# Performance work log

Hardware: AMD Instinct MI355X
Metric: run time of the kernel (lower is better)

Reference implementation:

```python
import math
import jax, jax.numpy as jnp
import numpy as np

E = 24  # num experts


def layer_norm(x, w, b, eps=1e-6):
    m = x.mean(-1, keepdims=True)
    v = x.var(-1, keepdims=True)
    return (x - m) / jnp.sqrt(v + eps) * w + b


def top2_dispatch(x, Wg, C):
    # x: [S, d] -> combine/dispatch: [S, E, C] (GShard/DeepSpeed top-2 gating)
    logits = x @ Wg                                   # [S, E]
    gates = jax.nn.softmax(logits, axis=-1)
    idx1 = jnp.argmax(gates, axis=-1)
    m1 = jax.nn.one_hot(idx1, E, dtype=x.dtype)       # [S, E]
    masked = jnp.where(m1 > 0, -jnp.inf, logits)
    idx2 = jnp.argmax(masked, axis=-1)
    m2 = jax.nn.one_hot(idx2, E, dtype=x.dtype)
    # position of each token within its expert's capacity buffer
    loc1 = jnp.cumsum(m1, axis=0) - m1
    loc2 = jnp.cumsum(m2, axis=0) - m2 + jnp.sum(m1, axis=0, keepdims=True)
    m1 = m1 * (loc1 < C)                              # drop overflow tokens
    m2 = m2 * (loc2 < C)
    g1 = jnp.sum(gates * m1, axis=-1)
    g2 = jnp.sum(gates * m2, axis=-1)
    denom = jnp.maximum(g1 + g2, 1e-9)
    g1, g2 = g1 / denom, g2 / denom
    p1 = jnp.sum(loc1 * m1, axis=-1).astype(jnp.int32)
    p2 = jnp.sum(loc2 * m2, axis=-1).astype(jnp.int32)
    c1 = g1[:, None, None] * m1[:, :, None] * jax.nn.one_hot(p1, C, dtype=x.dtype)[:, None, :]
    c2 = g2[:, None, None] * m2[:, :, None] * jax.nn.one_hot(p2, C, dtype=x.dtype)[:, None, :]
    combine = c1 + c2                                  # [S, E, C]
    dispatch = (combine > 0).astype(x.dtype)
    return combine, dispatch


def moe_apply(x, combine, dispatch, W, b):
    # dispatch tokens to expert buffers, per-expert GEMM, combine back
    disp = jnp.einsum('sec,sd->ecd', dispatch, x)      # [E, C, d]
    h = jnp.einsum('ecd,edf->ecf', disp, W) + b[:, None, :]
    return jnp.einsum('sec,ecf->sf', combine, h)       # [S, f]


def setup_inputs() -> dict:
    b, seq, d_in, d_hid = 4, 2048, 1024, 4096
    ks = jax.random.split(jax.random.key(0), 6)
    s = 0.02
    return {
        'x': jax.random.normal(ks[0], (b, seq, d_in), dtype=jnp.float32),
        'Wg': jax.random.normal(ks[1], (d_in, E), dtype=jnp.float32) * s,
        'W1': jax.random.normal(ks[2], (E, d_in, d_hid), dtype=jnp.float32) * s,
        'b1': jnp.zeros((E, d_hid), dtype=jnp.float32),
        'W2': jax.random.normal(ks[3], (E, d_hid, d_in), dtype=jnp.float32) * s,
        'b2': jnp.zeros((E, d_in), dtype=jnp.float32),
        'ln_hid_w': jnp.ones((4, d_hid), dtype=jnp.float32),
        'ln_hid_b': jnp.zeros((4, d_hid), dtype=jnp.float32),
        'ln_out_w': jnp.ones((d_in,), dtype=jnp.float32),
        'ln_out_b': jnp.zeros((d_in,), dtype=jnp.float32),
    }


def reference(x, Wg, W1, b1, W2, b2, ln_hid_w, ln_hid_b, ln_out_w, ln_out_b):
    bsz, seq, d = x.shape
    H = 4
    n = seq // H
    S = bsz * n  # tokens per sub-sequence MoE call
    C = math.ceil(2 * S / E)  # top-2 capacity, capacity_factor=1.0
    # b (h n) c -> h (b n) c
    xg = x.reshape(bsz, H, n, d).transpose(1, 0, 2, 3).reshape(H, S, d)

    def per_group(xf, lw, lb):
        combine, dispatch = top2_dispatch(xf, Wg, C)
        h = moe_apply(xf, combine, dispatch, W1, b1)       # [S, d_hid]
        h = layer_norm(h, lw, lb)
        h = jax.nn.relu(h)                                  # dropout = identity (eval)
        return moe_apply(h, combine, dispatch, W2, b2)      # reuse gate_decision

    out = jax.vmap(per_group)(xg, ln_hid_w, ln_hid_b)       # [H, S, d]
    out = out.reshape(H, bsz, n, d).transpose(1, 0, 2, 3).reshape(bsz, seq, d)
    return layer_norm(out + x, ln_out_w, ln_out_b)
```

## Files before the change

### kernel.cpp

```cpp
#include <hip/hip_runtime.h>
#include <cstdint>
#include <cstddef>

#define E_      24
#define D_IN    1024
#define D_HID   4096
#define HGRP    4
#define BSZ     4
#define SEQ     2048
#define NSUB    512
#define S_      2048
#define NTOKG   8192
#define CAP     171
#define MR      768
#define MTILE   3

typedef __attribute__((ext_vector_type(4))) float          f32x4;
typedef __attribute__((ext_vector_type(2))) float          f32x2;
typedef __attribute__((ext_vector_type(4))) unsigned short u16x4;
typedef __attribute__((ext_vector_type(8))) unsigned short u16x8;
typedef __attribute__((ext_vector_type(4))) unsigned int   u32x4;
typedef __attribute__((ext_vector_type(8))) short          s16x8;

__device__ __forceinline__ unsigned short f2bf(float f) {
  unsigned int u = __float_as_uint(f);
  u += 0x7fffu + ((u >> 16) & 1u);
  return (unsigned short)(u >> 16);
}
__device__ __forceinline__ float bf2f(unsigned short v) {
  return __uint_as_float(((unsigned int)v) << 16);
}

__global__ __launch_bounds__(64)
void k_gating(const float* __restrict__ x, const float* __restrict__ Wg,
              int* __restrict__ tokE1, int* __restrict__ tokE2,
              float* __restrict__ tokG1, float* __restrict__ tokG2) {
  int tg = blockIdx.x;
  int h = tg >> 11, s = tg & 2047;
  int bi = s >> 9, ni = s & 511;
  const float* xr = x + ((size_t)bi*SEQ + (size_t)h*NSUB + ni) * D_IN;
  int lane = threadIdx.x;
  float acc[E_];
  #pragma unroll
  for (int e = 0; e < E_; ++e) acc[e] = 0.f;
  #pragma unroll
  for (int it = 0; it < D_IN/256; ++it) {
    f32x4 xv = *(const f32x4*)(xr + it*256 + lane*4);
    #pragma unroll
    for (int j = 0; j < 4; ++j) {
      float xs = xv[j];
      const float* wrow = Wg + (size_t)(it*256 + lane*4 + j) * E_;
      #pragma unroll
      for (int e = 0; e < E_; ++e) acc[e] += xs * wrow[e];
    }
  }
  #pragma unroll
  for (int e = 0; e < E_; ++e) {
    float v = acc[e];
    v += __shfl_xor(v, 32); v += __shfl_xor(v, 16); v += __shfl_xor(v, 8);
    v += __shfl_xor(v, 4);  v += __shfl_xor(v, 2);  v += __shfl_xor(v, 1);
    acc[e] = v;
  }
  if (lane == 0) {
    float mx = acc[0];
    #pragma unroll
    for (int e = 1; e < E_; ++e) mx = fmaxf(mx, acc[e]);
    float den = 0.f;
    #pragma unroll
    for (int e = 0; e < E_; ++e) den += expf(acc[e] - mx);
    int i1 = 0; float v1 = acc[0];
    #pragma unroll
    for (int e = 1; e < E_; ++e) if (acc[e] > v1) { v1 = acc[e]; i1 = e; }
    int i2 = -1; float v2 = -3.4e38f;
    #pragma unroll
    for (int e = 0; e < E_; ++e) if (e != i1 && acc[e] > v2) { v2 = acc[e]; i2 = e; }
    tokE1[tg] = i1; tokE2[tg] = i2;
    tokG1[tg] = expf(v1 - mx) / den;
    tokG2[tg] = expf(v2 - mx) / den;
  }
}

__global__ void k_init_slots(int* __restrict__ slotTok) {
  slotTok[blockIdx.x*256 + threadIdx.x] = -1;
}

__global__ __launch_bounds__(64)
void k_scan(const int* __restrict__ tokE1, const int* __restrict__ tokE2,
            float* __restrict__ tokG1, float* __restrict__ tokG2,
            int* __restrict__ tokP1, int* __restrict__ tokP2,
            int* __restrict__ slotTok) {
  int h = blockIdx.x;
  int lane = threadIdx.x;
  __shared__ int cnt[64][E_];
  __shared__ int tot1[E_];
  const int CH = S_/64;
  const int* e1 = tokE1 + h*S_;
  const int* e2 = tokE2 + h*S_;
  #pragma unroll
  for (int e = 0; e < E_; ++e) cnt[lane][e] = 0;
  __syncthreads();
  for (int k = 0; k < CH; ++k) cnt[lane][e1[lane*CH + k]]++;
  __syncthreads();
  if (lane < E_) {
    int run = 0;
    for (int j = 0; j < 64; ++j) { int t = cnt[j][lane]; cnt[j][lane] = run; run += t; }
    tot1[lane] = run;
  }
  __syncthreads();
  for (int k = 0; k < CH; ++k) {
    int s = lane*CH + k;
    int e = e1[s];
    int p = cnt[lane][e]++;
    int tg = h*S_ + s;
    if (p < CAP) { tokP1[tg] = p; slotTok[e*MR + h*CAP + p] = tg; }
    else         { tokP1[tg] = -1; }
  }
  __syncthreads();
  #pragma unroll
  for (int e = 0; e < E_; ++e) cnt[lane][e] = 0;
  __syncthreads();
  for (int k = 0; k < CH; ++k) cnt[lane][e2[lane*CH + k]]++;
  __syncthreads();
  if (lane < E_) {
    int run = tot1[lane];
    for (int j = 0; j < 64; ++j) { int t = cnt[j][lane]; cnt[j][lane] = run; run += t; }
  }
  __syncthreads();
  for (int k = 0; k < CH; ++k) {
    int s = lane*CH + k;
    int e = e2[s];
    int p = cnt[lane][e]++;
    int tg = h*S_ + s;
    if (p < CAP) { tokP2[tg] = p; slotTok[e*MR + h*CAP + p] = tg; }
    else         { tokP2[tg] = -1; }
  }
  __syncthreads();
  for (int k = 0; k < CH; ++k) {
    int tg = h*S_ + k*64 + lane;
    float g1 = (tokP1[tg] >= 0) ? tokG1[tg] : 0.f;
    float g2 = (tokP2[tg] >= 0) ? tokG2[tg] : 0.f;
    float den = fmaxf(g1 + g2, 1e-9f);
    tokG1[tg] = g1 / den;
    tokG2[tg] = g2 / den;
  }
}

__global__ __launch_bounds__(256)
void k_gather1(const float* __restrict__ x, const int* __restrict__ slotTok,
               unsigned short* __restrict__ A1) {
  int row = blockIdx.x;
  int tok = slotTok[row];
  int t = threadIdx.x;
  int k = t*4;
  int ba = ((k & 63)*2) ^ ((row & 7) << 4);
  char* dst = (char*)A1 + (size_t)row*(D_IN*2) + (size_t)(k >> 6)*128 + ba;
  u16x4 pk;
  if (tok >= 0) {
    int h = tok >> 11, s = tok & 2047;
    int bi = s >> 9, ni = s & 511;
    const float* xr = x + ((size_t)bi*SEQ + (size_t)h*NSUB + ni) * D_IN;
    f32x4 v = *(const f32x4*)(xr + k);
    pk.x = f2bf(v.x); pk.y = f2bf(v.y); pk.z = f2bf(v.z); pk.w = f2bf(v.w);
  } else {
    pk.x = 0; pk.y = 0; pk.z = 0; pk.w = 0;
  }
  *(u16x4*)dst = pk;
}

template<int K, int N>
__global__ __launch_bounds__(512, 4)
void k_gemm(const unsigned short* __restrict__ A, const float* __restrict__ W,
            const float* __restrict__ bias, unsigned short* __restrict__ Out) {
  const int NT = N / 128;
  int cpx = gridDim.x >> 3;
  int lb = blockIdx.x;
  int bid = (lb & 7) * cpx + (lb >> 3);
  int mt  = bid % MTILE;
  int rem = bid / MTILE;
  int nt  = rem % NT;
  int e   = rem / NT;

  const char*  Ab = (const char*)A + ((size_t)e*MR + (size_t)mt*256) * (K*2);
  const float* We = W + (size_t)e*K*N + (size_t)nt*128;

  __shared__ unsigned short As[256*64];
  __shared__ unsigned short Bs[128*64];
  int tid  = threadIdx.x;
  int lane = tid & 63;
  int wid  = tid >> 6;
  int wr = wid >> 1, wc = wid & 1;

  f32x4 acc[4][4];
  #pragma unroll
  for (int i = 0; i < 4; ++i)
    #pragma unroll
    for (int j = 0; j < 4; ++j) acc[i][j] = (f32x4)0.f;

  int bn0 = (tid & 63) * 2;
  int bkh = (tid >> 6) * 8;
  f32x2 bPre[8];

  auto loadB = [&](int kt) {
    const float* p = We + (size_t)(kt*64 + bkh)*N + bn0;
    #pragma unroll
    for (int q = 0; q < 8; ++q) bPre[q] = *(const f32x2*)(p + (size_t)q*N);
  };
  auto storeB = [&]() {
    u16x8 c0, c1;
    #pragma unroll
    for (int q = 0; q < 8; ++q) { c0[q] = f2bf(bPre[q].x); c1[q] = f2bf(bPre[q].y); }
    int r0 = bn0, r1 = bn0 + 1;
    *(u16x8*)((char*)Bs + r0*128 + ((bkh*2) ^ ((r0 & 7) << 4))) = c0;
    *(u16x8*)((char*)Bs + r1*128 + ((bkh*2) ^ ((r1 & 7) << 4))) = c1;
  };
  auto stageA = [&](int kt) {
    #pragma unroll
    for (int i = 0; i < 4; ++i) {
      int L = i*8192 + tid*16;
      const char* src = Ab + (size_t)(L >> 7)*(K*2) + (size_t)kt*128 + (L & 127);
      __builtin_amdgcn_global_load_lds(
          (const __attribute__((address_space(1))) void*)src,
          (__attribute__((address_space(3))) void*)((char*)As + L),
          16, 0, 0);
    }
  };

  const int NKT = K / 64;
  loadB(0);
  for (int kt = 0; kt < NKT; ++kt) {
    __syncthreads();
    stageA(kt);
    storeB();
    __syncthreads();
    if (kt + 1 < NKT) loadB(kt + 1);
    #pragma unroll
    for (int kk = 0; kk < 2; ++kk) {
      s16x8 afr[4], bfr[4];
      int kx2 = (kk*32 + (lane >> 4)*8) * 2;
      #pragma unroll
      for (int i = 0; i < 4; ++i) {
        int row = wr*64 + i*16 + (lane & 15);
        afr[i] = *(const s16x8*)((const char*)As + row*128 + (kx2 ^ ((row & 7) << 4)));
        int col = wc*64 + i*16 + (lane & 15);
        bfr[i] = *(const s16x8*)((const char*)Bs + col*128 + (kx2 ^ ((col & 7) << 4)));
      }
      #pragma unroll
      for (int i = 0; i < 4; ++i)
        #pragma unroll
        for (int j = 0; j < 4; ++j)
          acc[i][j] = __builtin_amdgcn_mfma_f32_16x16x32_bf16(afr[i], bfr[j], acc[i][j], 0, 0, 0);
    }
  }
  #pragma unroll
  for (int j = 0; j < 4; ++j) {
    int col = nt*128 + wc*64 + j*16 + (lane & 15);
    float bv = bias[(size_t)e*N + col];
    #pragma unroll
    for (int i = 0; i < 4; ++i) {
      int rowb = mt*256 + wr*64 + i*16 + (lane >> 4)*4;
      #pragma unroll
      for (int r = 0; r < 4; ++r) {
        float v = acc[i][j][r] + bv;
        Out[(size_t)e*MR*N + (size_t)(rowb + r)*N + col] = f2bf(v);
      }
    }
  }
}

__global__ __launch_bounds__(256)
void k_zero_empty(const int* __restrict__ slotTok, unsigned short* __restrict__ A2) {
  int row = blockIdx.x;
  if (slotTok[row] >= 0) return;
  u32x4 z = (u32x4)0u;
  char* base = (char*)A2 + (size_t)row*(D_HID*2) + threadIdx.x*32;
  *(u32x4*)base = z;
  *(u32x4*)(base + 16) = z;
}

__global__ __launch_bounds__(256)
void k_combine_ln(const unsigned short* __restrict__ H1,
                  const int* __restrict__ tokE1, const int* __restrict__ tokE2,
                  const int* __restrict__ tokP1, const int* __restrict__ tokP2,
                  const float* __restrict__ tokG1, const float* __restrict__ tokG2,
                  const float* __restrict__ lnw, const float* __restrict__ lnb,
                  unsigned short* __restrict__ A2) {
  int tg = blockIdx.x;
  int h = tg >> 11;
  int p1 = tokP1[tg], p2 = tokP2[tg];
  if (p1 < 0 && p2 < 0) return;
  float g1 = tokG1[tg], g2 = tokG2[tg];
  long r1 = (p1 >= 0) ? ((long)tokE1[tg]*MR + h*CAP + p1) : -1;
  long r2 = (p2 >= 0) ? ((long)tokE2[tg]*MR + h*CAP + p2) : -1;
  int t = threadIdx.x;
  float v[16];
  float sum = 0.f, sq = 0.f;
  #pragma unroll
  for (int u = 0; u < 4; ++u) {
    int f = u*1024 + t*4;
    float a0 = 0.f, a1 = 0.f, a2 = 0.f, a3 = 0.f;
    if (r1 >= 0) {
      u16x4 q = *(const u16x4*)(H1 + (size_t)r1*D_HID + f);
      a0 += g1*bf2f(q.x); a1 += g1*bf2f(q.y); a2 += g1*bf2f(q.z); a3 += g1*bf2f(q.w);
    }
    if (r2 >= 0) {
      u16x4 q = *(const u16x4*)(H1 + (size_t)r2*D_HID + f);
      a0 += g2*bf2f(q.x); a1 += g2*bf2f(q.y); a2 += g2*bf2f(q.z); a3 += g2*bf2f(q.w);
    }
    v[u*4+0] = a0; v[u*4+1] = a1; v[u*4+2] = a2; v[u*4+3] = a3;
    sum += a0 + a1 + a2 + a3;
    sq  += a0*a0 + a1*a1 + a2*a2 + a3*a3;
  }
  #pragma unroll
  for (int o = 32; o; o >>= 1) { sum += __shfl_xor(sum, o); sq += __shfl_xor(sq, o); }
  __shared__ float redA[4], redB[4];
  int wid = t >> 6;
  if ((t & 63) == 0) { redA[wid] = sum; redB[wid] = sq; }
  __syncthreads();
  float S = redA[0] + redA[1] + redA[2] + redA[3];
  float Q = redB[0] + redB[1] + redB[2] + redB[3];
  float m = S * (1.f / D_HID);
  float var = Q * (1.f / D_HID) - m*m;
  float rs = rsqrtf(var + 1e-6f);
  #pragma unroll
  for (int u = 0; u < 4; ++u) {
    int f = u*1024 + t*4;
    u16x4 pk;
    float y0 = fmaxf((v[u*4+0]-m)*rs*lnw[h*D_HID+f+0] + lnb[h*D_HID+f+0], 0.f);
    float y1 = fmaxf((v[u*4+1]-m)*rs*lnw[h*D_HID+f+1] + lnb[h*D_HID+f+1], 0.f);
    float y2 = fmaxf((v[u*4+2]-m)*rs*lnw[h*D_HID+f+2] + lnb[h*D_HID+f+2], 0.f);
    float y3 = fmaxf((v[u*4+3]-m)*rs*lnw[h*D_HID+f+3] + lnb[h*D_HID+f+3], 0.f);
    pk.x = f2bf(y0); pk.y = f2bf(y1); pk.z = f2bf(y2); pk.w = f2bf(y3);
    int chunk = f >> 6;
    int ob = (f & 63)*2;
    if (r1 >= 0)
      *(u16x4*)((char*)A2 + (size_t)r1*(D_HID*2) + (size_t)chunk*128 + (ob ^ (((int)r1 & 7) << 4))) = pk;
    if (r2 >= 0)
      *(u16x4*)((char*)A2 + (size_t)r2*(D_HID*2) + (size_t)chunk*128 + (ob ^ (((int)r2 & 7) << 4))) = pk;
  }
}

__global__ __launch_bounds__(256)
void k_final(const unsigned short* __restrict__ H2, const float* __restrict__ x,
             const int* __restrict__ tokE1, const int* __restrict__ tokE2,
             const int* __restrict__ tokP1, const int* __restrict__ tokP2,
             const float* __restrict__ tokG1, const float* __restrict__ tokG2,
             const float* __restrict__ lnw, const float* __restrict__ lnb,
             float* __restrict__ out) {
  int tg = blockIdx.x;
  int h = tg >> 11, s = tg & 2047;
  int bi = s >> 9, ni = s & 511;
  size_t xoff = ((size_t)bi*SEQ + (size_t)h*NSUB + ni) * D_IN;
  int p1 = tokP1[tg], p2 = tokP2[tg];
  float g1 = tokG1[tg], g2 = tokG2[tg];
  int t = threadIdx.x;
  int f = t*4;
  f32x4 xv = *(const f32x4*)(x + xoff + f);
  float v0 = xv.x, v1 = xv.y, v2 = xv.z, v3 = xv.w;
  if (p1 >= 0) {
    size_t r1 = (size_t)tokE1[tg]*MR + h*CAP + p1;
    u16x4 q = *(const u16x4*)(H2 + r1*D_IN + f);
    v0 += g1*bf2f(q.x); v1 += g1*bf2f(q.y); v2 += g1*bf2f(q.z); v3 += g1*bf2f(q.w);
  }
  if (p2 >= 0) {
    size_t r2 = (size_t)tokE2[tg]*MR + h*CAP + p2;
    u16x4 q = *(const u16x4*)(H2 + r2*D_IN + f);
    v0 += g2*bf2f(q.x); v1 += g2*bf2f(q.y); v2 += g2*bf2f(q.z); v3 += g2*bf2f(q.w);
  }
  float sum = v0+v1+v2+v3, sq = v0*v0+v1*v1+v2*v2+v3*v3;
  #pragma unroll
  for (int o = 32; o; o >>= 1) { sum += __shfl_xor(sum, o); sq += __shfl_xor(sq, o); }
  __shared__ float redA[4], redB[4];
  int wid = t >> 6;
  if ((t & 63) == 0) { redA[wid] = sum; redB[wid] = sq; }
  __syncthreads();
  float S = redA[0] + redA[1] + redA[2] + redA[3];
  float Q = redB[0] + redB[1] + redB[2] + redB[3];
  float m = S * (1.f / D_IN);
  float var = Q * (1.f / D_IN) - m*m;
  float rs = rsqrtf(var + 1e-6f);
  f32x4 res;
  res.x = (v0 - m)*rs*lnw[f+0] + lnb[f+0];
  res.y = (v1 - m)*rs*lnw[f+1] + lnb[f+1];
  res.z = (v2 - m)*rs*lnw[f+2] + lnb[f+2];
  res.w = (v3 - m)*rs*lnw[f+3] + lnb[f+3];
  *(f32x4*)(out + xoff + f) = res;
}

extern "C" void kernel_launch(void* const* d_in, const int* in_sizes, int n_in,
                              void* d_out, int out_size, void* d_ws, size_t ws_size,
                              hipStream_t stream) {
  const float* x    = (const float*)d_in[0];
  const float* Wg   = (const float*)d_in[1];
  const float* W1   = (const float*)d_in[2];
  const float* b1   = (const float*)d_in[3];
  const float* W2   = (const float*)d_in[4];
  const float* b2   = (const float*)d_in[5];
  const float* lnhw = (const float*)d_in[6];
  const float* lnhb = (const float*)d_in[7];
  const float* lnow = (const float*)d_in[8];
  const float* lnob = (const float*)d_in[9];
  float* out = (float*)d_out;
  (void)in_sizes; (void)n_in; (void)out_size; (void)ws_size;

  char* ws = (char*)d_ws;
  size_t off = 0;
  auto take = [&](size_t bytes) -> char* {
    char* p = ws + off;
    off += (bytes + 255) & ~(size_t)255;
    return p;
  };
  int*   tokE1 = (int*)take(NTOKG*sizeof(int));
  int*   tokE2 = (int*)take(NTOKG*sizeof(int));
  int*   tokP1 = (int*)take(NTOKG*sizeof(int));
  int*   tokP2 = (int*)take(NTOKG*sizeof(int));
  float* tokG1 = (float*)take(NTOKG*sizeof(float));
  float* tokG2 = (float*)take(NTOKG*sizeof(float));
  int*   slotTok = (int*)take((size_t)E_*MR*sizeof(int));
  unsigned short* A1 = (unsigned short*)take((size_t)E_*MR*D_IN*2);
  unsigned short* H1 = (unsigned short*)take((size_t)E_*MR*D_HID*2);
  unsigned short* A2 = (unsigned short*)take((size_t)E_*MR*D_HID*2);
  unsigned short* H2 = (unsigned short*)take((size_t)E_*MR*D_IN*2);

  k_init_slots<<<dim3(E_*MR/256), dim3(256), 0, stream>>>(slotTok);
  k_gating<<<dim3(NTOKG), dim3(64), 0, stream>>>(x, Wg, tokE1, tokE2, tokG1, tokG2);
  k_scan<<<dim3(HGRP), dim3(64), 0, stream>>>(tokE1, tokE2, tokG1, tokG2, tokP1, tokP2, slotTok);
  k_gather1<<<dim3(E_*MR), dim3(256), 0, stream>>>(x, slotTok, A1);
  k_gemm<D_IN, D_HID><<<dim3(E_*(D_HID/128)*MTILE), dim3(512), 0, stream>>>(A1, W1, b1, H1);
  k_zero_empty<<<dim3(E_*MR), dim3(256), 0, stream>>>(slotTok, A2);
  k_combine_ln<<<dim3(NTOKG), dim3(256), 0, stream>>>(H1, tokE1, tokE2, tokP1, tokP2,
                                                      tokG1, tokG2, lnhw, lnhb, A2);
  k_gemm<D_HID, D_IN><<<dim3(E_*(D_IN/128)*MTILE), dim3(512), 0, stream>>>(A2, W2, b2, H2);
  k_final<<<dim3(NTOKG), dim3(256), 0, stream>>>(H2, x, tokE1, tokE2, tokP1, tokP2,
                                                 tokG1, tokG2, lnow, lnob, out);
}
```

Measured before the change: 812.4 us.

## Double-buffer LDS tiles in expert GEMM with manual waitcnt ping-pong

```diff
diff --git a/kernel.cpp b/kernel.cpp
--- a/kernel.cpp
+++ b/kernel.cpp
@@ -168,7 +168,7 @@
 }
 
 template<int K, int N>
-__global__ __launch_bounds__(512, 4)
+__global__ __launch_bounds__(512)
 void k_gemm(const unsigned short* __restrict__ A, const float* __restrict__ W,
             const float* __restrict__ bias, unsigned short* __restrict__ Out) {
   const int NT = N / 128;
@@ -183,8 +183,10 @@
   const char*  Ab = (const char*)A + ((size_t)e*MR + (size_t)mt*256) * (K*2);
   const float* We = W + (size_t)e*K*N + (size_t)nt*128;
 
-  __shared__ unsigned short As[256*64];
-  __shared__ unsigned short Bs[128*64];
+  __shared__ unsigned short As0[256*64];
+  __shared__ unsigned short As1[256*64];
+  __shared__ unsigned short Bs0[128*64];
+  __shared__ unsigned short Bs1[128*64];
   int tid  = threadIdx.x;
   int lane = tid & 63;
   int wid  = tid >> 6;
@@ -198,22 +200,22 @@
 
   int bn0 = (tid & 63) * 2;
   int bkh = (tid >> 6) * 8;
-  f32x2 bPre[8];
-
-  auto loadB = [&](int kt) {
+  f32x2 bPreA[8], bPreB[8];
+
+  auto loadB = [&](int kt, f32x2* bp) {
     const float* p = We + (size_t)(kt*64 + bkh)*N + bn0;
     #pragma unroll
-    for (int q = 0; q < 8; ++q) bPre[q] = *(const f32x2*)(p + (size_t)q*N);
+    for (int q = 0; q < 8; ++q) bp[q] = *(const f32x2*)(p + (size_t)q*N);
   };
-  auto storeB = [&]() {
+  auto storeB = [&](const f32x2* bp, unsigned short* Bs) {
     u16x8 c0, c1;
     #pragma unroll
-    for (int q = 0; q < 8; ++q) { c0[q] = f2bf(bPre[q].x); c1[q] = f2bf(bPre[q].y); }
+    for (int q = 0; q < 8; ++q) { c0[q] = f2bf(bp[q].x); c1[q] = f2bf(bp[q].y); }
     int r0 = bn0, r1 = bn0 + 1;
     *(u16x8*)((char*)Bs + r0*128 + ((bkh*2) ^ ((r0 & 7) << 4))) = c0;
     *(u16x8*)((char*)Bs + r1*128 + ((bkh*2) ^ ((r1 & 7) << 4))) = c1;
   };
-  auto stageA = [&](int kt) {
+  auto stageA = [&](int kt, unsigned short* As) {
     #pragma unroll
     for (int i = 0; i < 4; ++i) {
       int L = i*8192 + tid*16;
@@ -224,15 +226,7 @@
           16, 0, 0);
     }
   };
-
-  const int NKT = K / 64;
-  loadB(0);
-  for (int kt = 0; kt < NKT; ++kt) {
-    __syncthreads();
-    stageA(kt);
-    storeB();
-    __syncthreads();
-    if (kt + 1 < NKT) loadB(kt + 1);
+  auto compute = [&](const unsigned short* As, const unsigned short* Bs) {
     #pragma unroll
     for (int kk = 0; kk < 2; ++kk) {
       s16x8 afr[4], bfr[4];
@@ -250,6 +244,28 @@
         for (int j = 0; j < 4; ++j)
           acc[i][j] = __builtin_amdgcn_mfma_f32_16x16x32_bf16(afr[i], bfr[j], acc[i][j], 0, 0, 0);
     }
+  };
+
+  const int NKT = K / 64;
+  stageA(0, As0); loadB(0, bPreA);
+  for (int kt = 0; kt < NKT; kt += 2) {
+    stageA(kt + 1, As1);
+    loadB(kt + 1, bPreB);
+    storeB(bPreA, Bs0);
+    asm volatile("s_waitcnt vmcnt(12) lgkmcnt(0)" ::: "memory");
+    __builtin_amdgcn_sched_barrier(0);
+    __builtin_amdgcn_s_barrier();
+    compute(As0, Bs0);
+    __builtin_amdgcn_sched_barrier(0);
+    __builtin_amdgcn_s_barrier();
+    if (kt + 2 < NKT) { stageA(kt + 2, As0); loadB(kt + 2, bPreA); }
+    storeB(bPreB, Bs1);
+    asm volatile("s_waitcnt vmcnt(12) lgkmcnt(0)" ::: "memory");
+    __builtin_amdgcn_sched_barrier(0);
+    __builtin_amdgcn_s_barrier();
+    compute(As1, Bs1);
+    __builtin_amdgcn_sched_barrier(0);
+    __builtin_amdgcn_s_barrier();
   }
   #pragma unroll
   for (int j = 0; j < 4; ++j) {
```

New measurement: 944.8 us. +16.3%, slower.

## Widen expert GEMM tile to 256x256 with double-buffered LDS pipeline

Applied to the files above, without the earlier changes.

```diff
diff --git a/kernel.cpp b/kernel.cpp
--- a/kernel.cpp
+++ b/kernel.cpp
@@ -168,10 +168,10 @@
 }
 
 template<int K, int N>
-__global__ __launch_bounds__(512, 4)
+__global__ __launch_bounds__(512, 2)
 void k_gemm(const unsigned short* __restrict__ A, const float* __restrict__ W,
             const float* __restrict__ bias, unsigned short* __restrict__ Out) {
-  const int NT = N / 128;
+  const int NT = N / 256;
   int cpx = gridDim.x >> 3;
   int lb = blockIdx.x;
   int bid = (lb & 7) * cpx + (lb >> 3);
@@ -181,83 +181,119 @@
   int e   = rem / NT;
 
   const char*  Ab = (const char*)A + ((size_t)e*MR + (size_t)mt*256) * (K*2);
-  const float* We = W + (size_t)e*K*N + (size_t)nt*128;
-
-  __shared__ unsigned short As[256*64];
-  __shared__ unsigned short Bs[128*64];
+  const float* We = W + (size_t)e*K*N + (size_t)nt*256;
+
+  __shared__ unsigned short As0[256*64];
+  __shared__ unsigned short As1[256*64];
+  __shared__ unsigned short Bs0[256*64];
+  __shared__ unsigned short Bs1[256*64];
+
   int tid  = threadIdx.x;
   int lane = tid & 63;
   int wid  = tid >> 6;
-  int wr = wid >> 1, wc = wid & 1;
-
-  f32x4 acc[4][4];
-  #pragma unroll
-  for (int i = 0; i < 4; ++i)
+  int wr = wid >> 2, wc = wid & 3;
+
+  f32x4 acc[8][4];
+  #pragma unroll
+  for (int i = 0; i < 8; ++i)
     #pragma unroll
     for (int j = 0; j < 4; ++j) acc[i][j] = (f32x4)0.f;
 
-  int bn0 = (tid & 63) * 2;
-  int bkh = (tid >> 6) * 8;
-  f32x2 bPre[8];
+  int cB  = tid & 127;
+  int bkh = (tid >> 7) * 16;
+  float w0[16], w1[16];
 
   auto loadB = [&](int kt) {
-    const float* p = We + (size_t)(kt*64 + bkh)*N + bn0;
-    #pragma unroll
-    for (int q = 0; q < 8; ++q) bPre[q] = *(const f32x2*)(p + (size_t)q*N);
-  };
-  auto storeB = [&]() {
-    u16x8 c0, c1;
-    #pragma unroll
-    for (int q = 0; q < 8; ++q) { c0[q] = f2bf(bPre[q].x); c1[q] = f2bf(bPre[q].y); }
-    int r0 = bn0, r1 = bn0 + 1;
-    *(u16x8*)((char*)Bs + r0*128 + ((bkh*2) ^ ((r0 & 7) << 4))) = c0;
-    *(u16x8*)((char*)Bs + r1*128 + ((bkh*2) ^ ((r1 & 7) << 4))) = c1;
-  };
-  auto stageA = [&](int kt) {
-    #pragma unroll
-    for (int i = 0; i < 4; ++i) {
+    const float* p = We + (size_t)(kt*64 + bkh)*N + cB;
+    #pragma unroll
+    for (int q = 0; q < 16; ++q) { w0[q] = p[(size_t)q*N]; w1[q] = p[(size_t)q*N + 128]; }
+  };
+  auto storeB = [&](unsigned short* Bs) {
+    #pragma unroll
+    for (int h = 0; h < 2; ++h) {
+      u16x8 c0, c1;
+      #pragma unroll
+      for (int q = 0; q < 8; ++q) { c0[q] = f2bf(w0[h*8+q]); c1[q] = f2bf(w1[h*8+q]); }
+      int kbb = bkh*2 + 16*h;
+      int n0 = cB, n1 = cB + 128;
+      *(u16x8*)((char*)Bs + n0*128 + (kbb ^ ((n0 & 7) << 4))) = c0;
+      *(u16x8*)((char*)Bs + n1*128 + (kbb ^ ((n1 & 7) << 4))) = c1;
+    }
+  };
+  auto stageA = [&](int kt, int half, unsigned short* As) {
+    #pragma unroll
+    for (int i = 0; i < 2; ++i) {
       int L = i*8192 + tid*16;
-      const char* src = Ab + (size_t)(L >> 7)*(K*2) + (size_t)kt*128 + (L & 127);
+      const char* src = Ab + (size_t)(half*128 + (L >> 7))*(K*2) + (size_t)kt*128 + (L & 127);
       __builtin_amdgcn_global_load_lds(
           (const __attribute__((address_space(1))) void*)src,
-          (__attribute__((address_space(3))) void*)((char*)As + L),
+          (__attribute__((address_space(3))) void*)((char*)As + half*16384 + L),
           16, 0, 0);
     }
   };
-
+  auto dsFrags = [&](const unsigned short* As, const unsigned short* Bs,
+                     int ra, int ks, s16x8* afr, s16x8* bfr) {
+    int kb = ks*64 + (lane >> 4)*16;
+    #pragma unroll
+    for (int i = 0; i < 4; ++i) {
+      int r = wr*128 + ra*64 + i*16 + (lane & 15);
+      afr[i] = *(const s16x8*)((const char*)As + r*128 + (kb ^ ((r & 7) << 4)));
+      int c = wc*64 + i*16 + (lane & 15);
+      bfr[i] = *(const s16x8*)((const char*)Bs + c*128 + (kb ^ ((c & 7) << 4)));
+    }
+  };
+  auto mfmaQ = [&](int ra, const s16x8* afr, const s16x8* bfr) {
+    __builtin_amdgcn_s_setprio(1);
+    #pragma unroll
+    for (int i = 0; i < 4; ++i)
+      #pragma unroll
+      for (int j = 0; j < 4; ++j)
+        acc[ra*4+i][j] = __builtin_amdgcn_mfma_f32_16x16x32_bf16(afr[i], bfr[j], acc[ra*4+i][j], 0, 0, 0);
+    __builtin_amdgcn_s_setprio(0);
+  };
+
+  unsigned short *Acur = As0, *Anxt = As1, *Bcur = Bs0, *Bnxt = Bs1;
   const int NKT = K / 64;
+
+  stageA(0, 0, Acur); stageA(0, 1, Acur);
   loadB(0);
+  storeB(Bcur);
+  asm volatile("s_waitcnt vmcnt(0)" ::: "memory");
+  __syncthreads();
+
   for (int kt = 0; kt < NKT; ++kt) {
+    int ktn = (kt + 1 < NKT) ? kt + 1 : NKT - 1;
+    s16x8 afr[4], bfr[4];
+    dsFrags(Acur, Bcur, 0, 0, afr, bfr);
+    stageA(ktn, 0, Anxt);
+    __builtin_amdgcn_s_barrier();
+    mfmaQ(0, afr, bfr);
+    dsFrags(Acur, Bcur, 1, 0, afr, bfr);
+    loadB(ktn);
+    __builtin_amdgcn_sched_barrier(0);
+    __builtin_amdgcn_s_barrier();
+    mfmaQ(1, afr, bfr);
+    dsFrags(Acur, Bcur, 0, 1, afr, bfr);
+    stageA(ktn, 1, Anxt);
+    __builtin_amdgcn_s_barrier();
+    mfmaQ(0, afr, bfr);
+    dsFrags(Acur, Bcur, 1, 1, afr, bfr);
+    __builtin_amdgcn_s_barrier();
+    mfmaQ(1, afr, bfr);
+    storeB(Bnxt);
+    asm volatile("s_waitcnt vmcnt(0)" ::: "memory");
     __syncthreads();
-    stageA(kt);
-    storeB();
-    __syncthreads();
-    if (kt + 1 < NKT) loadB(kt + 1);
-    #pragma unroll
-    for (int kk = 0; kk < 2; ++kk) {
-      s16x8 afr[4], bfr[4];
-      int kx2 = (kk*32 + (lane >> 4)*8) * 2;
-      #pragma unroll
-      for (int i = 0; i < 4; ++i) {
-        int row = wr*64 + i*16 + (lane & 15);
-        afr[i] = *(const s16x8*)((const char*)As + row*128 + (kx2 ^ ((row & 7) << 4)));
-        int col = wc*64 + i*16 + (lane & 15);
-        bfr[i] = *(const s16x8*)((const char*)Bs + col*128 + (kx2 ^ ((col & 7) << 4)));
-      }
-      #pragma unroll
-      for (int i = 0; i < 4; ++i)
-        #pragma unroll
-        for (int j = 0; j < 4; ++j)
-          acc[i][j] = __builtin_amdgcn_mfma_f32_16x16x32_bf16(afr[i], bfr[j], acc[i][j], 0, 0, 0);
-    }
-  }
+    unsigned short* t1 = Acur; Acur = Anxt; Anxt = t1;
+    unsigned short* t2 = Bcur; Bcur = Bnxt; Bnxt = t2;
+  }
+
   #pragma unroll
   for (int j = 0; j < 4; ++j) {
-    int col = nt*128 + wc*64 + j*16 + (lane & 15);
+    int col = nt*256 + wc*64 + j*16 + (lane & 15);
     float bv = bias[(size_t)e*N + col];
     #pragma unroll
-    for (int i = 0; i < 4; ++i) {
-      int rowb = mt*256 + wr*64 + i*16 + (lane >> 4)*4;
+    for (int i = 0; i < 8; ++i) {
+      int rowb = mt*256 + wr*128 + i*16 + (lane >> 4)*4;
       #pragma unroll
       for (int r = 0; r < 4; ++r) {
         float v = acc[i][j][r] + bv;
@@ -425,11 +461,11 @@
   k_gating<<<dim3(NTOKG), dim3(64), 0, stream>>>(x, Wg, tokE1, tokE2, tokG1, tokG2);
   k_scan<<<dim3(HGRP), dim3(64), 0, stream>>>(tokE1, tokE2, tokG1, tokG2, tokP1, tokP2, slotTok);
   k_gather1<<<dim3(E_*MR), dim3(256), 0, stream>>>(x, slotTok, A1);
-  k_gemm<D_IN, D_HID><<<dim3(E_*(D_HID/128)*MTILE), dim3(512), 0, stream>>>(A1, W1, b1, H1);
+  k_gemm<D_IN, D_HID><<<dim3(E_*(D_HID/256)*MTILE), dim3(512), 0, stream>>>(A1, W1, b1, H1);
   k_zero_empty<<<dim3(E_*MR), dim3(256), 0, stream>>>(slotTok, A2);
   k_combine_ln<<<dim3(NTOKG), dim3(256), 0, stream>>>(H1, tokE1, tokE2, tokP1, tokP2,
                                                       tokG1, tokG2, lnhw, lnhb, A2);
-  k_gemm<D_HID, D_IN><<<dim3(E_*(D_IN/128)*MTILE), dim3(512), 0, stream>>>(A2, W2, b2, H2);
+  k_gemm<D_HID, D_IN><<<dim3(E_*(D_IN/256)*MTILE), dim3(512), 0, stream>>>(A2, W2, b2, H2);
   k_final<<<dim3(NTOKG), dim3(256), 0, stream>>>(H2, x, tokE1, tokE2, tokP1, tokP2,
                                                  tokG1, tokG2, lnow, lnob, out);
 }
```

Result: slower. 855.1 us (+5.3%).

## Shrink GEMM tile to 128x128 with 256 threads and double-buffered W loads

Applied to the files above, without the earlier changes.

```diff
diff --git a/kernel.cpp b/kernel.cpp
--- a/kernel.cpp
+++ b/kernel.cpp
@@ -13,10 +13,9 @@
 #define NTOKG   8192
 #define CAP     171
 #define MR      768
-#define MTILE   3
+#define MTILE   6
 
 typedef __attribute__((ext_vector_type(4))) float          f32x4;
-typedef __attribute__((ext_vector_type(2))) float          f32x2;
 typedef __attribute__((ext_vector_type(4))) unsigned short u16x4;
 typedef __attribute__((ext_vector_type(8))) unsigned short u16x8;
 typedef __attribute__((ext_vector_type(4))) unsigned int   u32x4;
@@ -167,11 +166,12 @@
   *(u16x4*)dst = pk;
 }
 
-template<int K, int N>
-__global__ __launch_bounds__(512, 4)
+template<int KROW, int N>
+__global__ __launch_bounds__(256)
 void k_gemm(const unsigned short* __restrict__ A, const float* __restrict__ W,
             const float* __restrict__ bias, unsigned short* __restrict__ Out) {
   const int NT = N / 128;
+  const int NKT = KROW / 64;
   int cpx = gridDim.x >> 3;
   int lb = blockIdx.x;
   int bid = (lb & 7) * cpx + (lb >> 3);
@@ -180,11 +180,12 @@
   int nt  = rem % NT;
   int e   = rem / NT;
 
-  const char*  Ab = (const char*)A + ((size_t)e*MR + (size_t)mt*256) * (K*2);
-  const float* We = W + (size_t)e*K*N + (size_t)nt*128;
-
-  __shared__ unsigned short As[256*64];
+  const char*  Ab = (const char*)A + ((size_t)e*MR + (size_t)mt*128) * (KROW*2);
+  const float* We = W + (size_t)e*KROW*N + (size_t)nt*128;
+
+  __shared__ unsigned short As[128*64];
   __shared__ unsigned short Bs[128*64];
+
   int tid  = threadIdx.x;
   int lane = tid & 63;
   int wid  = tid >> 6;
@@ -196,43 +197,35 @@
     #pragma unroll
     for (int j = 0; j < 4; ++j) acc[i][j] = (f32x4)0.f;
 
-  int bn0 = (tid & 63) * 2;
-  int bkh = (tid >> 6) * 8;
-  f32x2 bPre[8];
-
-  auto loadB = [&](int kt) {
-    const float* p = We + (size_t)(kt*64 + bkh)*N + bn0;
-    #pragma unroll
-    for (int q = 0; q < 8; ++q) bPre[q] = *(const f32x2*)(p + (size_t)q*N);
+  int bn = (tid & 31) * 4;
+  int bk = (tid >> 5) * 8;
+  f32x4 rA[8], rB[8];
+
+  auto loadB = [&](int kt, f32x4* wv) {
+    const float* p = We + (size_t)(kt*64 + bk)*N + bn;
+    #pragma unroll
+    for (int q = 0; q < 8; ++q) wv[q] = *(const f32x4*)(p + (size_t)q*N);
   };
-  auto storeB = [&]() {
-    u16x8 c0, c1;
-    #pragma unroll
-    for (int q = 0; q < 8; ++q) { c0[q] = f2bf(bPre[q].x); c1[q] = f2bf(bPre[q].y); }
-    int r0 = bn0, r1 = bn0 + 1;
-    *(u16x8*)((char*)Bs + r0*128 + ((bkh*2) ^ ((r0 & 7) << 4))) = c0;
-    *(u16x8*)((char*)Bs + r1*128 + ((bkh*2) ^ ((r1 & 7) << 4))) = c1;
+  auto writeB = [&](const f32x4* wv) {
+    #pragma unroll
+    for (int c = 0; c < 4; ++c) {
+      u16x8 col;
+      #pragma unroll
+      for (int q = 0; q < 8; ++q) col[q] = f2bf(wv[q][c]);
+      int n = bn + c;
+      *(u16x8*)((char*)Bs + n*128 + ((bk*2) ^ ((n & 7) << 4))) = col;
+    }
   };
   auto stageA = [&](int kt) {
     #pragma unroll
     for (int i = 0; i < 4; ++i) {
-      int L = i*8192 + tid*16;
-      const char* src = Ab + (size_t)(L >> 7)*(K*2) + (size_t)kt*128 + (L & 127);
+      int L = i*4096 + tid*16;
       __builtin_amdgcn_global_load_lds(
-          (const __attribute__((address_space(1))) void*)src,
-          (__attribute__((address_space(3))) void*)((char*)As + L),
-          16, 0, 0);
+          (const __attribute__((address_space(1))) void*)(Ab + (size_t)(L >> 7)*(KROW*2) + (size_t)kt*128 + (L & 127)),
+          (__attribute__((address_space(3))) void*)((char*)As + L), 16, 0, 0);
     }
   };
-
-  const int NKT = K / 64;
-  loadB(0);
-  for (int kt = 0; kt < NKT; ++kt) {
-    __syncthreads();
-    stageA(kt);
-    storeB();
-    __syncthreads();
-    if (kt + 1 < NKT) loadB(kt + 1);
+  auto compute = [&]() {
     #pragma unroll
     for (int kk = 0; kk < 2; ++kk) {
       s16x8 afr[4], bfr[4];
@@ -250,14 +243,31 @@
         for (int j = 0; j < 4; ++j)
           acc[i][j] = __builtin_amdgcn_mfma_f32_16x16x32_bf16(afr[i], bfr[j], acc[i][j], 0, 0, 0);
     }
-  }
+  };
+
+  loadB(0, rA);
+  for (int kt = 0; kt < NKT; kt += 2) {
+    __syncthreads();
+    stageA(kt);
+    writeB(rA);
+    __syncthreads();
+    loadB(kt + 1, rB);
+    compute();
+    __syncthreads();
+    stageA(kt + 1);
+    writeB(rB);
+    __syncthreads();
+    if (kt + 2 < NKT) loadB(kt + 2, rA);
+    compute();
+  }
+
   #pragma unroll
   for (int j = 0; j < 4; ++j) {
     int col = nt*128 + wc*64 + j*16 + (lane & 15);
     float bv = bias[(size_t)e*N + col];
     #pragma unroll
     for (int i = 0; i < 4; ++i) {
-      int rowb = mt*256 + wr*64 + i*16 + (lane >> 4)*4;
+      int rowb = mt*128 + wr*64 + i*16 + (lane >> 4)*4;
       #pragma unroll
       for (int r = 0; r < 4; ++r) {
         float v = acc[i][j][r] + bv;
@@ -425,11 +435,11 @@
   k_gating<<<dim3(NTOKG), dim3(64), 0, stream>>>(x, Wg, tokE1, tokE2, tokG1, tokG2);
   k_scan<<<dim3(HGRP), dim3(64), 0, stream>>>(tokE1, tokE2, tokG1, tokG2, tokP1, tokP2, slotTok);
   k_gather1<<<dim3(E_*MR), dim3(256), 0, stream>>>(x, slotTok, A1);
-  k_gemm<D_IN, D_HID><<<dim3(E_*(D_HID/128)*MTILE), dim3(512), 0, stream>>>(A1, W1, b1, H1);
+  k_gemm<D_IN, D_HID><<<dim3(E_*(D_HID/128)*MTILE), dim3(256), 0, stream>>>(A1, W1, b1, H1);
   k_zero_empty<<<dim3(E_*MR), dim3(256), 0, stream>>>(slotTok, A2);
   k_combine_ln<<<dim3(NTOKG), dim3(256), 0, stream>>>(H1, tokE1, tokE2, tokP1, tokP2,
                                                       tokG1, tokG2, lnhw, lnhb, A2);
-  k_gemm<D_HID, D_IN><<<dim3(E_*(D_IN/128)*MTILE), dim3(512), 0, stream>>>(A2, W2, b2, H2);
+  k_gemm<D_HID, D_IN><<<dim3(E_*(D_IN/128)*MTILE), dim3(256), 0, stream>>>(A2, W2, b2, H2);
   k_final<<<dim3(NTOKG), dim3(256), 0, stream>>>(H2, x, tokE1, tokE2, tokP1, tokP2,
                                                  tokG1, tokG2, lnow, lnob, out);
 }
```

Result: slower. 891.8 us (+9.8%).
